# Performance work log

Measured on AMD Instinct MI355X. Metric: run time of the kernel, lower is better.

Reference implementation:

```python
import jax, jax.numpy as jnp
import numpy as np

N, E = 50000, 800000
D, H, C, ED = 128, 8, 16, 4  # embed_dim, heads, head_dim, edge_dim


def _add_self_loops(edge_index, ea, n):
    # PyG add_self_loops with fill_value='mean': self-loop edge_attr is the
    # mean of incoming edge attributes per destination node (0 if none).
    src, dst = edge_index[0], edge_index[1]
    deg = jax.ops.segment_sum(jnp.ones((src.shape[0],), ea.dtype), dst, num_segments=n)
    loop_ea = jax.ops.segment_sum(ea, dst, num_segments=n) / jnp.maximum(deg, 1.0)[:, None]
    ar = jnp.arange(n, dtype=src.dtype)
    return (jnp.concatenate([src, ar]), jnp.concatenate([dst, ar]),
            jnp.concatenate([ea, loop_ea], axis=0))


def _gatv2(x, src, dst, ea, Wl, bl, Wr, br, We, att, bias, concat):
    n = x.shape[0]
    xl = (x @ Wl + bl).reshape(n, H, C)   # lin_l -> messages (source)
    xr = (x @ Wr + br).reshape(n, H, C)   # lin_r -> target
    e = (ea @ We).reshape(-1, H, C)       # lin_edge (no bias in PyG)
    m = jax.nn.leaky_relu(xl[src] + xr[dst] + e, negative_slope=0.2)  # [Etot,H,C]
    alpha = jnp.einsum('ehc,hc->eh', m, att)
    amax = jax.ops.segment_max(alpha, dst, num_segments=n)   # every node has a self loop
    ex = jnp.exp(alpha - amax[dst])
    den = jax.ops.segment_sum(ex, dst, num_segments=n)
    a = ex / den[dst]                                        # segment softmax over dst
    out = jax.ops.segment_sum(xl[src] * a[:, :, None], dst, num_segments=n)  # [N,H,C]
    out = out.reshape(n, H * C) if concat else out.mean(axis=1)
    return out + bias


def _ln(h, g, b):
    mu = h.mean(-1, keepdims=True)
    var = jnp.var(h, axis=-1, keepdims=True)
    return (h - mu) / jnp.sqrt(var + 1e-5) * g + b


def setup_inputs() -> dict:
    key = jax.random.key(0)
    ks = jax.random.split(key, 32)
    s = 0.05
    inp = {
        'x': jax.random.normal(ks[0], (N, D), jnp.float32),
        'edge_index': jax.random.randint(ks[1], (2, E), 0, N, jnp.int32),
        'edge_attr': jax.random.normal(ks[2], (E, ED), jnp.float32),
    }
    dims = [(D, H * C), (H * C, H * C), (H * C, C)]  # (in_dim, bias_dim per layer)
    k = 3
    for i, (din, bdim) in enumerate(dims):
        inp[f'Wl{i}'] = jax.random.normal(ks[k], (din, H * C), jnp.float32) * s; k += 1
        inp[f'bl{i}'] = jnp.zeros((H * C,), jnp.float32)
        inp[f'Wr{i}'] = jax.random.normal(ks[k], (din, H * C), jnp.float32) * s; k += 1
        inp[f'br{i}'] = jnp.zeros((H * C,), jnp.float32)
        inp[f'We{i}'] = jax.random.normal(ks[k], (ED, H * C), jnp.float32) * s; k += 1
        inp[f'att{i}'] = jax.random.normal(ks[k], (H, C), jnp.float32) * s; k += 1
        inp[f'b{i}'] = jnp.zeros((bdim,), jnp.float32)
        inp[f'g{i}'] = jnp.ones((bdim,), jnp.float32)
        inp[f'be{i}'] = jnp.zeros((bdim,), jnp.float32)
    inp['Wout'] = jax.random.normal(ks[k], (C, D), jnp.float32) * s
    inp['bout'] = jnp.zeros((D,), jnp.float32)
    return inp


def reference(x, edge_index, edge_attr,
              Wl0, bl0, Wr0, br0, We0, att0, b0, g0, be0,
              Wl1, bl1, Wr1, br1, We1, att1, b1, g1, be1,
              Wl2, bl2, Wr2, br2, We2, att2, b2, g2, be2,
              Wout, bout):
    n = x.shape[0]
    src, dst, ea = _add_self_loops(edge_index, edge_attr, n)
    layers = [
        (Wl0, bl0, Wr0, br0, We0, att0, b0, g0, be0, True),
        (Wl1, bl1, Wr1, br1, We1, att1, b1, g1, be1, True),
        (Wl2, bl2, Wr2, br2, We2, att2, b2, g2, be2, False),
    ]
    for (Wl, bl, Wr, br, We, att, bias, g, be, concat) in layers:
        h = _gatv2(x, src, dst, ea, Wl, bl, Wr, br, We, att, bias, concat)
        h = jax.nn.elu(h)
        h = _ln(h, g, be)
        if h.shape == x.shape:  # residual (layers 0,1)
            h = h + x
        x = h
    return x @ Wout + bout
```

## Files before the change

kernel.cpp:

```cpp
#include <hip/hip_runtime.h>
#include <hip/hip_bf16.h>

#define ND 128
#define NH 8
#define NC 16

typedef float v2f __attribute__((ext_vector_type(2)));
typedef short bf16x8 __attribute__((ext_vector_type(8)));
typedef float f32x4 __attribute__((ext_vector_type(4)));

static inline size_t alignup(size_t x){ return (x + 255) & ~size_t(255); }

__device__ __forceinline__ ushort f2bf(float f){
    __hip_bfloat16 h = __float2bfloat16(f);
    return *reinterpret_cast<ushort*>(&h);
}

__device__ __forceinline__ v2f unpack_bf2(uint u){
    v2f r;
    r.x = __uint_as_float(u << 16);
    r.y = __uint_as_float(u & 0xffff0000u);
    return r;
}

__device__ __forceinline__ v2f lrelu2(v2f z){
    v2f s = z * 0.2f;
    v2f r;
    r.x = fmaxf(z.x, s.x);
    r.y = fmaxf(z.y, s.y);
    return r;
}

__device__ __forceinline__ float hred8(float x){
    int y;
    y = __builtin_amdgcn_mov_dpp(__float_as_int(x), 0xB1, 0xF, 0xF, true);
    x += __int_as_float(y);
    y = __builtin_amdgcn_mov_dpp(__float_as_int(x), 0x4E, 0xF, 0xF, true);
    x += __int_as_float(y);
    y = __builtin_amdgcn_mov_dpp(__float_as_int(x), 0x141, 0xF, 0xF, true);
    x += __int_as_float(y);
    return x;
}


__global__ void hist_kernel(const int* __restrict__ dsts, int* __restrict__ deg, int E)
{
    int e = blockIdx.x * blockDim.x + threadIdx.x;
    if (e >= E) return;
    atomicAdd(&deg[dsts[e]], 1);
}

__global__ __launch_bounds__(1024) void scan_kernel(const int* __restrict__ deg,
                                                    int* __restrict__ rowstart, int n)
{
    __shared__ int wsum[16];
    int tid = threadIdx.x;
    int lane = tid & 63, wid = tid >> 6;
    int carry = 0;
    for (int base = 0; base < n; base += 4096) {
        int idx = base + tid * 4;
        int4 d = make_int4(0, 0, 0, 0);
        if (idx + 3 < n) d = *(const int4*)(deg + idx);
        else {
            if (idx < n)     d.x = deg[idx];
            if (idx + 1 < n) d.y = deg[idx + 1];
            if (idx + 2 < n) d.z = deg[idx + 2];
        }
        int p0 = (d.x + 3) & ~3, p1 = (d.y + 3) & ~3;
        int p2 = (d.z + 3) & ~3, p3 = (d.w + 3) & ~3;
        int tsum = p0 + p1 + p2 + p3;
        int s = tsum;
        #pragma unroll
        for (int o = 1; o < 64; o <<= 1) {
            int t = __shfl_up(s, o);
            if (lane >= o) s += t;
        }
        if (lane == 63) wsum[wid] = s;
        __syncthreads();
        int off = carry;
        #pragma unroll
        for (int w = 0; w < 16; ++w) {
            int ws_ = wsum[w];
            if (w < wid) off += ws_;
        }
        int total = 0;
        #pragma unroll
        for (int w = 0; w < 16; ++w) total += wsum[w];
        int excl = off + (s - tsum);
        if (idx < n)     rowstart[idx]     = excl;
        if (idx + 1 < n) rowstart[idx + 1] = excl + p0;
        if (idx + 2 < n) rowstart[idx + 2] = excl + p0 + p1;
        if (idx + 3 < n) rowstart[idx + 3] = excl + p0 + p1 + p2;
        carry += total;
        __syncthreads();
    }
    if (tid == 0) rowstart[n] = carry;
}

__global__ void scatter_kernel(const int* __restrict__ srcs, const int* __restrict__ dsts,
                               const float4* __restrict__ ea4,
                               const int* __restrict__ rowstart, int* __restrict__ cursor,
                               int* __restrict__ srcb_sorted, uint2* __restrict__ eab_sorted, int E)
{
    int e = blockIdx.x * blockDim.x + threadIdx.x;
    if (e >= E) return;
    int d = dsts[e];
    int pos = rowstart[d] + atomicAdd(&cursor[d], 1);
    srcb_sorted[pos] = srcs[e] << 8;
    float4 a = ea4[e];
    uint2 p;
    p.x = (uint)f2bf(a.x) | ((uint)f2bf(a.y) << 16);
    p.y = (uint)f2bf(a.z) | ((uint)f2bf(a.w) << 16);
    eab_sorted[pos] = p;
}

__global__ void padfill_kernel(const int* __restrict__ rowstart, const int* __restrict__ deg,
                               int* __restrict__ srcb_sorted, uint2* __restrict__ eab_sorted, int n)
{
    int v = blockIdx.x * blockDim.x + threadIdx.x;
    if (v < n) {
        int d = deg[v];
        int p = rowstart[v] + d;
        int pe = rowstart[v] + ((d + 3) & ~3);
        for (; p < pe; ++p) {
            srcb_sorted[p] = 0;
            eab_sorted[p] = make_uint2(0u, 0u);
        }
    } else if (v < n + 64) {
        int p = rowstart[n] + (v - n);
        srcb_sorted[p] = 0;
        eab_sorted[p] = make_uint2(0u, 0u);
    }
}

__global__ void easum_kernel(const int* __restrict__ rowstart, const int* __restrict__ deg,
                             const uint2* __restrict__ eab_sorted, float4* __restrict__ easum, int n)
{
    int v = blockIdx.x * blockDim.x + threadIdx.x;
    if (v >= n) return;
    int p0 = rowstart[v], d = deg[v];
    float sx = 0.f, sy = 0.f, sz = 0.f, sw = 0.f;
    for (int p = p0; p < p0 + d; ++p) {
        uint2 a = eab_sorted[p];
        sx += __uint_as_float(a.x << 16);
        sy += __uint_as_float(a.x & 0xffff0000u);
        sz += __uint_as_float(a.y << 16);
        sw += __uint_as_float(a.y & 0xffff0000u);
    }
    float inv = 1.0f / (float)(d > 0 ? d : 1);
    easum[v] = make_float4(sx * inv, sy * inv, sz * inv, sw * inv);
}


struct WSrc { const float* p[6]; };

__global__ void wconv_kernel(WSrc s, ushort* __restrict__ wt)
{
    int id = blockIdx.x * blockDim.x + threadIdx.x;
    int m = id >> 14;
    int r = id & 16383;
    int n = r >> 7, k = r & 127;
    wt[(size_t)m * 16384 + n * 128 + k] = f2bf(s.p[m][k * 128 + n]);
}


__global__ __launch_bounds__(256) void gemm_mfma(
    const float* __restrict__ X,
    const ushort* __restrict__ WTl, const float* __restrict__ bl,
    const ushort* __restrict__ WTr, const float* __restrict__ br,
    ushort* __restrict__ XLB, ushort* __restrict__ XRB, int nrows)
{
    __shared__ ushort xhi[64][136];
    __shared__ ushort xlo[64][136];
    int tid = threadIdx.x;
    int row0 = blockIdx.x * 64;

    const float4* X4 = (const float4*)X;
    #pragma unroll
    for (int i = tid; i < 64*32; i += 256) {
        int r = i >> 5, c = i & 31;
        float4 v = make_float4(0.f, 0.f, 0.f, 0.f);
        if (row0 + r < nrows) v = X4[(size_t)(row0 + r) * 32 + c];
        ushort4 h, l;
        h.x = f2bf(v.x); l.x = f2bf(v.x - __uint_as_float((uint)h.x << 16));
        h.y = f2bf(v.y); l.y = f2bf(v.y - __uint_as_float((uint)h.y << 16));
        h.z = f2bf(v.z); l.z = f2bf(v.z - __uint_as_float((uint)h.z << 16));
        h.w = f2bf(v.w); l.w = f2bf(v.w - __uint_as_float((uint)h.w << 16));
        *(ushort4*)&xhi[r][c * 4] = h;
        *(ushort4*)&xlo[r][c * 4] = l;
    }
    __syncthreads();

    int lane = tid & 63;
    int wid = tid >> 6;
    int c15 = lane & 15;
    int kblk = lane >> 4;
    int rowb = wid * 16;

    f32x4 accl[8], accr[8];
    #pragma unroll
    for (int nt = 0; nt < 8; ++nt) {
        float bvl = bl[nt * 16 + c15];
        float bvr = br[nt * 16 + c15];
        accl[nt] = (f32x4){bvl, bvl, bvl, bvl};
        accr[nt] = (f32x4){bvr, bvr, bvr, bvr};
    }

    const bf16x8* WL8 = (const bf16x8*)WTl;
    const bf16x8* WR8 = (const bf16x8*)WTr;

    #pragma unroll
    for (int kc = 0; kc < 4; ++kc) {
        int k0 = kc * 32 + kblk * 8;
        bf16x8 ahi = *(const bf16x8*)&xhi[rowb + c15][k0];
        bf16x8 alo = *(const bf16x8*)&xlo[rowb + c15][k0];
        int kidx = k0 >> 3;
        #pragma unroll
        for (int nt = 0; nt < 8; ++nt) {
            int bi = (nt * 16 + c15) * 16 + kidx;
            bf16x8 bfl = WL8[bi];
            bf16x8 bfr = WR8[bi];
            accl[nt] = __builtin_amdgcn_mfma_f32_16x16x32_bf16(ahi, bfl, accl[nt], 0, 0, 0);
            accl[nt] = __builtin_amdgcn_mfma_f32_16x16x32_bf16(alo, bfl, accl[nt], 0, 0, 0);
            accr[nt] = __builtin_amdgcn_mfma_f32_16x16x32_bf16(ahi, bfr, accr[nt], 0, 0, 0);
            accr[nt] = __builtin_amdgcn_mfma_f32_16x16x32_bf16(alo, bfr, accr[nt], 0, 0, 0);
        }
    }

    int crow = rowb + (lane >> 4) * 4;
    #pragma unroll
    for (int j = 0; j < 4; ++j) {
        int row = row0 + crow + j;
        if (row < nrows) {
            #pragma unroll
            for (int nt = 0; nt < 8; ++nt) {
                XLB[(size_t)row * 128 + nt * 16 + c15] = f2bf(accl[nt][j]);
                XRB[(size_t)row * 128 + nt * 16 + c15] = f2bf(accr[nt][j]);
            }
        }
    }
}


__device__ __forceinline__ void gat_wave(
    int dstv, int t,
    const uint* __restrict__ xl_u, const uint* __restrict__ xr_u,
    const int* __restrict__ rowstart, const int* __restrict__ deg,
    const int* __restrict__ srcb_sorted, const uint2* __restrict__ eab_sorted,
    const float4* __restrict__ easum,
    const float* __restrict__ We, const float* __restrict__ att,
    v2f& r_out, float& l_out)
{
    v2f we0  = ((const v2f*)(We))[t];
    v2f we1  = ((const v2f*)(We + ND))[t];
    v2f we2  = ((const v2f*)(We + 2*ND))[t];
    v2f we3  = ((const v2f*)(We + 3*ND))[t];
    v2f attv = ((const v2f*)att)[t] * 1.44269504f;
    v2f xrv  = unpack_bf2(xr_u[(((uint)dstv) << 6) + t]);

    int p0 = __builtin_amdgcn_readfirstlane(rowstart[dstv]);
    int dv = __builtin_amdgcn_readfirstlane(deg[dstv]);
    int nb = (dv + 3) >> 2;

    uint xsw = xl_u[(((uint)dstv) << 6) + t];

    const int* sp = srcb_sorted + p0;
    const uint4* ebp = (const uint4*)(eab_sorted + p0);
    const char* xlc = (const char*)xl_u;
    uint t4 = (uint)t * 4u;

    v2f a = {0.f, 0.f};
    float lsum = 0.f;

    int4 s0 = *(const int4*)(sp);
    uint xA0 = *(const uint*)(xlc + ((uint)s0.x + t4));
    uint xA1 = *(const uint*)(xlc + ((uint)s0.y + t4));
    uint xA2 = *(const uint*)(xlc + ((uint)s0.z + t4));
    uint xA3 = *(const uint*)(xlc + ((uint)s0.w + t4));
    int4 s1 = *(const int4*)(sp + 4);
    uint xB0 = *(const uint*)(xlc + ((uint)s1.x + t4));
    uint xB1 = *(const uint*)(xlc + ((uint)s1.y + t4));
    uint xB2 = *(const uint*)(xlc + ((uint)s1.z + t4));
    uint xB3 = *(const uint*)(xlc + ((uint)s1.w + t4));
    int4 s2 = *(const int4*)(sp + 8);
    uint xC0 = *(const uint*)(xlc + ((uint)s2.x + t4));
    uint xC1 = *(const uint*)(xlc + ((uint)s2.y + t4));
    uint xC2 = *(const uint*)(xlc + ((uint)s2.z + t4));
    uint xC3 = *(const uint*)(xlc + ((uint)s2.w + t4));
    int4 s3 = *(const int4*)(sp + 12);
    uint4 eA = ebp[0];
    uint4 eB = ebp[1];

    for (int ib = 0; ib < nb; ++ib) {
        uint xD0 = *(const uint*)(xlc + ((uint)s3.x + t4));
        uint xD1 = *(const uint*)(xlc + ((uint)s3.y + t4));
        uint xD2 = *(const uint*)(xlc + ((uint)s3.z + t4));
        uint xD3 = *(const uint*)(xlc + ((uint)s3.w + t4));
        int4 s4 = *(const int4*)(sp + ib*4 + 16);
        uint4 eNA = ebp[(ib + 1) * 2];
        uint4 eNB = ebp[(ib + 1) * 2 + 1];

        float e0x = __uint_as_float(eA.x << 16), e0y = __uint_as_float(eA.x & 0xffff0000u);
        float e0z = __uint_as_float(eA.y << 16), e0w = __uint_as_float(eA.y & 0xffff0000u);
        float e1x = __uint_as_float(eA.z << 16), e1y = __uint_as_float(eA.z & 0xffff0000u);
        float e1z = __uint_as_float(eA.w << 16), e1w = __uint_as_float(eA.w & 0xffff0000u);
        float e2x = __uint_as_float(eB.x << 16), e2y = __uint_as_float(eB.x & 0xffff0000u);
        float e2z = __uint_as_float(eB.y << 16), e2w = __uint_as_float(eB.y & 0xffff0000u);
        float e3x = __uint_as_float(eB.z << 16), e3y = __uint_as_float(eB.z & 0xffff0000u);
        float e3z = __uint_as_float(eB.w << 16), e3w = __uint_as_float(eB.w & 0xffff0000u);

        v2f b0 = xrv + we0*e0x + we1*e0y + we2*e0z + we3*e0w;
        v2f b1 = xrv + we0*e1x + we1*e1y + we2*e1z + we3*e1w;
        v2f b2 = xrv + we0*e2x + we1*e2y + we2*e2z + we3*e2w;
        v2f b3 = xrv + we0*e3x + we1*e3y + we2*e3z + we3*e3w;

        v2f x0 = unpack_bf2(xA0);
        v2f x1 = unpack_bf2(xA1);
        v2f x2 = unpack_bf2(xA2);
        v2f x3 = unpack_bf2(xA3);

        v2f l0 = lrelu2(x0 + b0);
        v2f l1 = lrelu2(x1 + b1);
        v2f l2 = lrelu2(x2 + b2);
        v2f l3 = lrelu2(x3 + b3);

        v2f q0 = l0 * attv;
        v2f q1 = l1 * attv;
        v2f q2 = l2 * attv;
        v2f q3 = l3 * attv;
        float pt0 = q0.x + q0.y;
        float pt1 = q1.x + q1.y;
        float pt2 = q2.x + q2.y;
        float pt3 = q3.x + q3.y;

        if (ib == nb - 1) {
            int live = dv - ib*4;
            pt1 = (live > 1) ? pt1 : -1e30f;
            pt2 = (live > 2) ? pt2 : -1e30f;
            pt3 = (live > 3) ? pt3 : -1e30f;
        }

        float al0 = hred8(pt0);
        float al1 = hred8(pt1);
        float al2 = hred8(pt2);
        float al3 = hred8(pt3);

        float pe0 = exp2f(al0);
        float pe1 = exp2f(al1);
        float pe2 = exp2f(al2);
        float pe3 = exp2f(al3);
        lsum += (pe0 + pe1) + (pe2 + pe3);
        a += x0 * pe0;
        a += x1 * pe1;
        a += x2 * pe2;
        a += x3 * pe3;

        xA0 = xB0; xA1 = xB1; xA2 = xB2; xA3 = xB3;
        xB0 = xC0; xB1 = xC1; xB2 = xC2; xB3 = xC3;
        xC0 = xD0; xC1 = xD1; xC2 = xD2; xC3 = xD3;
        s3 = s4;
        eA = eNA; eB = eNB;
    }

    float4 em = easum[dstv];
    v2f xs = unpack_bf2(xsw);
    v2f bs = xrv + we0*em.x + we1*em.y + we2*em.z + we3*em.w;
    v2f ls = lrelu2(xs + bs);
    v2f qs = ls * attv;
    float al = hred8(qs.x + qs.y);
    float pe = exp2f(al);
    l_out = lsum + pe;
    r_out = a + xs * pe;
}

__global__ __launch_bounds__(256) void attn_concat(
    const ushort* __restrict__ xlb, const ushort* __restrict__ xrb,
    const float* __restrict__ xin,
    const int* __restrict__ rowstart, const int* __restrict__ deg,
    const int* __restrict__ srcb_sorted, const uint2* __restrict__ eab_sorted,
    const float4* __restrict__ easum,
    const float* __restrict__ We, const float* __restrict__ att,
    const float* __restrict__ bias, const float* __restrict__ g, const float* __restrict__ be,
    float* __restrict__ out, int n)
{
    int wid = threadIdx.x >> 6;
    int t = threadIdx.x & 63;
    int dstv = blockIdx.x * 4 + wid;
    if (dstv >= n) return;

    v2f av; float l;
    gat_wave(dstv, t, (const uint*)xlb, (const uint*)xrb, rowstart, deg, srcb_sorted,
             eab_sorted, easum, We, att, av, l);

    v2f bv = ((const v2f*)bias)[t];
    float linv = 1.0f / l;
    v2f h = av * linv + bv;
    h.x = h.x > 0.f ? h.x : (__expf(h.x) - 1.0f);
    h.y = h.y > 0.f ? h.y : (__expf(h.y) - 1.0f);

    float ss = h.x + h.y, qq = h.x*h.x + h.y*h.y;
    #pragma unroll
    for (int o = 1; o < 64; o <<= 1) { ss += __shfl_xor(ss, o); qq += __shfl_xor(qq, o); }
    float mu = ss * (1.0f / ND);
    float var = qq * (1.0f / ND) - mu * mu;
    float rstd = rsqrtf(var + 1e-5f);

    v2f gv  = ((const v2f*)g)[t];
    v2f bev = ((const v2f*)be)[t];
    v2f xiv = ((const v2f*)(xin + (size_t)dstv * ND))[t];
    v2f o2 = (h - mu) * rstd * gv + bev + xiv;
    ((v2f*)(out + (size_t)dstv * ND))[t] = o2;
}

__global__ __launch_bounds__(256) void attn_final(
    const ushort* __restrict__ xlb, const ushort* __restrict__ xrb,
    const int* __restrict__ rowstart, const int* __restrict__ deg,
    const int* __restrict__ srcb_sorted, const uint2* __restrict__ eab_sorted,
    const float4* __restrict__ easum,
    const float* __restrict__ We, const float* __restrict__ att,
    const float* __restrict__ b2, const float* __restrict__ g2, const float* __restrict__ be2,
    const float* __restrict__ Wout, const float* __restrict__ bout,
    float* __restrict__ out, int n)
{
    __shared__ float h16s[4][16];
    int wid = threadIdx.x >> 6;
    int t = threadIdx.x & 63;
    int dstv = blockIdx.x * 4 + wid;
    if (dstv >= n) return;

    v2f av; float l;
    gat_wave(dstv, t, (const uint*)xlb, (const uint*)xrb, rowstart, deg, srcb_sorted,
             eab_sorted, easum, We, att, av, l);
    float linv = 1.0f / l;
    float v0 = av.x * linv, v1 = av.y * linv;

    #pragma unroll
    for (int o = 8; o < 64; o <<= 1) { v0 += __shfl_xor(v0, o); v1 += __shfl_xor(v1, o); }
    int cc = t & 7;
    float2 b2v = ((const float2*)b2)[cc];
    v0 = v0 * (1.0f / NH) + b2v.x;
    v1 = v1 * (1.0f / NH) + b2v.y;
    v0 = v0 > 0.f ? v0 : (__expf(v0) - 1.0f);
    v1 = v1 > 0.f ? v1 : (__expf(v1) - 1.0f);

    float ss = v0 + v1, qq = v0*v0 + v1*v1;
    #pragma unroll
    for (int o = 1; o < 8; o <<= 1) { ss += __shfl_xor(ss, o); qq += __shfl_xor(qq, o); }
    float mu = ss * (1.0f / NC);
    float var = qq * (1.0f / NC) - mu * mu;
    float rstd = rsqrtf(var + 1e-5f);
    float2 g2v = ((const float2*)g2)[cc];
    float2 be2v = ((const float2*)be2)[cc];
    float t0 = (v0 - mu) * rstd * g2v.x + be2v.x;
    float t1 = (v1 - mu) * rstd * g2v.y + be2v.y;

    if (t < 8) { h16s[wid][2*t] = t0; h16s[wid][2*t + 1] = t1; }

    float2 ov = ((const float2*)bout)[t];
    #pragma unroll
    for (int k = 0; k < NC; k++) {
        float hk = h16s[wid][k];
        float2 wv = ((const float2*)Wout)[k * 64 + t];
        ov.x = fmaf(hk, wv.x, ov.x);
        ov.y = fmaf(hk, wv.y, ov.y);
    }
    ((float2*)(out + (size_t)dstv * ND))[t] = ov;
}


extern "C" void kernel_launch(void* const* d_in, const int* in_sizes, int n_in,
                              void* d_out, int out_size, void* d_ws, size_t ws_size,
                              hipStream_t stream)
{
    const float* x_in = (const float*)d_in[0];
    const int*   ei   = (const int*)d_in[1];
    const float* ea   = (const float*)d_in[2];
    const int N = in_sizes[0] / ND;
    const int E = in_sizes[1] / 2;
    const int* srcs = ei;
    const int* dsts = ei + E;
    const float4* ea4 = (const float4*)ea;

    const float *Wl[3], *bl[3], *Wr[3], *br[3], *We[3], *att[3], *bb[3], *gg[3], *be[3];
    for (int l = 0; l < 3; l++) {
        int b = 3 + 9 * l;
        Wl[l]  = (const float*)d_in[b + 0];
        bl[l]  = (const float*)d_in[b + 1];
        Wr[l]  = (const float*)d_in[b + 2];
        br[l]  = (const float*)d_in[b + 3];
        We[l]  = (const float*)d_in[b + 4];
        att[l] = (const float*)d_in[b + 5];
        bb[l]  = (const float*)d_in[b + 6];
        gg[l]  = (const float*)d_in[b + 7];
        be[l]  = (const float*)d_in[b + 8];
    }
    const float* Wout = (const float*)d_in[30];
    const float* bout = (const float*)d_in[31];

    const size_t EP = (size_t)E + 3 * (size_t)N + 96;

    char* ws = (char*)d_ws;
    size_t off = 0;
    int* deg        = (int*)(ws + off);      off = alignup(off + (size_t)N * 4);
    int* cursor     = (int*)(ws + off);      off = alignup(off + (size_t)N * 4);
    size_t zero_bytes = off;
    int* rowstart   = (int*)(ws + off);      off = alignup(off + (size_t)(N + 1) * 4);
    int* srcb_sorted = (int*)(ws + off);     off = alignup(off + EP * 4);
    uint2* eab_sorted = (uint2*)(ws + off);  off = alignup(off + EP * 8);
    float4* easum   = (float4*)(ws + off);   off = alignup(off + (size_t)N * 16);
    ushort* xlb     = (ushort*)(ws + off);   off = alignup(off + (size_t)N * ND * 2);
    ushort* xrb     = (ushort*)(ws + off);   off = alignup(off + (size_t)N * ND * 2);
    float* xa       = (float*)(ws + off);    off = alignup(off + (size_t)N * ND * 4);
    ushort* wt      = (ushort*)(ws + off);   off = alignup(off + (size_t)6 * 16384 * 2);
    float* xb       = (float*)d_out;

    hipMemsetAsync(d_ws, 0, zero_bytes, stream);

    WSrc wsrc;
    wsrc.p[0] = Wl[0]; wsrc.p[1] = Wr[0];
    wsrc.p[2] = Wl[1]; wsrc.p[3] = Wr[1];
    wsrc.p[4] = Wl[2]; wsrc.p[5] = Wr[2];
    wconv_kernel<<<(6 * 16384) / 256, 256, 0, stream>>>(wsrc, wt);

    int ethreads = 256;
    int eblocks = (E + ethreads - 1) / ethreads;
    hist_kernel<<<eblocks, ethreads, 0, stream>>>(dsts, deg, E);
    scan_kernel<<<1, 1024, 0, stream>>>(deg, rowstart, N);
    padfill_kernel<<<(N + 64 + 255) / 256, 256, 0, stream>>>(rowstart, deg, srcb_sorted, eab_sorted, N);
    scatter_kernel<<<eblocks, ethreads, 0, stream>>>(srcs, dsts, ea4, rowstart, cursor,
                                                     srcb_sorted, eab_sorted, E);
    easum_kernel<<<(N + 255) / 256, 256, 0, stream>>>(rowstart, deg, eab_sorted, easum, N);

    int gblocks = (N + 63) / 64;
    int ablocks = (N + 3) / 4;

    const ushort* WT0l = wt;
    const ushort* WT0r = wt + 16384;
    const ushort* WT1l = wt + 2 * 16384;
    const ushort* WT1r = wt + 3 * 16384;
    const ushort* WT2l = wt + 4 * 16384;
    const ushort* WT2r = wt + 5 * 16384;

    gemm_mfma<<<gblocks, 256, 0, stream>>>(x_in, WT0l, bl[0], WT0r, br[0], xlb, xrb, N);
    attn_concat<<<ablocks, 256, 0, stream>>>(xlb, xrb, x_in, rowstart, deg, srcb_sorted, eab_sorted,
                                             easum, We[0], att[0], bb[0], gg[0], be[0], xa, N);
    gemm_mfma<<<gblocks, 256, 0, stream>>>(xa, WT1l, bl[1], WT1r, br[1], xlb, xrb, N);
    attn_concat<<<ablocks, 256, 0, stream>>>(xlb, xrb, xa, rowstart, deg, srcb_sorted, eab_sorted,
                                             easum, We[1], att[1], bb[1], gg[1], be[1], xb, N);
    gemm_mfma<<<gblocks, 256, 0, stream>>>(xb, WT2l, bl[2], WT2r, br[2], xlb, xrb, N);
    attn_final<<<ablocks, 256, 0, stream>>>(xlb, xrb, rowstart, deg, srcb_sorted, eab_sorted,
                                            easum, We[2], att[2], bb[2], gg[2], be[2],
                                            Wout, bout, (float*)d_out, N);
}
```

Baseline: 420.0 us.

## Pack edge records into uint4 AoS and make attention kernels persistent grid-stride

Merges the separate sorted source-index and bf16 edge-attribute arrays into a single 16-byte record per edge, so each edge's source and attributes arrive in one vector load. The gather pipeline is rewritten around these records, with prefetch indices clamped to the last block instead of reading into padding. The attention kernels become persistent: a fixed grid of 2048 blocks strides over nodes and hoists the per-lane weight, att, bias and norm parameter loads out of the node loop. The cost is a larger edge buffer (16 bytes per edge versus 12) that includes an unused word, plus clamping arithmetic in the inner loop.

```diff
diff --git a/kernel.cpp b/kernel.cpp
--- a/kernel.cpp
+++ b/kernel.cpp
@@ -10,6 +10,7 @@
 typedef float f32x4 __attribute__((ext_vector_type(4)));
 
 static inline size_t alignup(size_t x){ return (x + 255) & ~size_t(255); }
+__device__ __forceinline__ int imin(int a, int b){ return a < b ? a : b; }
 
 __device__ __forceinline__ ushort f2bf(float f){
     __hip_bfloat16 h = __float2bfloat16(f);
@@ -100,52 +101,46 @@
 __global__ void scatter_kernel(const int* __restrict__ srcs, const int* __restrict__ dsts,
                                const float4* __restrict__ ea4,
                                const int* __restrict__ rowstart, int* __restrict__ cursor,
-                               int* __restrict__ srcb_sorted, uint2* __restrict__ eab_sorted, int E)
+                               uint4* __restrict__ recs, int E)
 {
     int e = blockIdx.x * blockDim.x + threadIdx.x;
     if (e >= E) return;
     int d = dsts[e];
     int pos = rowstart[d] + atomicAdd(&cursor[d], 1);
-    srcb_sorted[pos] = srcs[e] << 8;
     float4 a = ea4[e];
-    uint2 p;
-    p.x = (uint)f2bf(a.x) | ((uint)f2bf(a.y) << 16);
-    p.y = (uint)f2bf(a.z) | ((uint)f2bf(a.w) << 16);
-    eab_sorted[pos] = p;
+    uint ea01 = (uint)f2bf(a.x) | ((uint)f2bf(a.y) << 16);
+    uint ea23 = (uint)f2bf(a.z) | ((uint)f2bf(a.w) << 16);
+    recs[pos] = make_uint4((uint)(srcs[e] << 8), ea01, ea23, 0u);
 }
 
 __global__ void padfill_kernel(const int* __restrict__ rowstart, const int* __restrict__ deg,
-                               int* __restrict__ srcb_sorted, uint2* __restrict__ eab_sorted, int n)
+                               uint4* __restrict__ recs, int n)
 {
     int v = blockIdx.x * blockDim.x + threadIdx.x;
     if (v < n) {
         int d = deg[v];
         int p = rowstart[v] + d;
         int pe = rowstart[v] + ((d + 3) & ~3);
-        for (; p < pe; ++p) {
-            srcb_sorted[p] = 0;
-            eab_sorted[p] = make_uint2(0u, 0u);
-        }
+        for (; p < pe; ++p) recs[p] = make_uint4(0u, 0u, 0u, 0u);
     } else if (v < n + 64) {
         int p = rowstart[n] + (v - n);
-        srcb_sorted[p] = 0;
-        eab_sorted[p] = make_uint2(0u, 0u);
+        recs[p] = make_uint4(0u, 0u, 0u, 0u);
     }
 }
 
 __global__ void easum_kernel(const int* __restrict__ rowstart, const int* __restrict__ deg,
-                             const uint2* __restrict__ eab_sorted, float4* __restrict__ easum, int n)
+                             const uint4* __restrict__ recs, float4* __restrict__ easum, int n)
 {
     int v = blockIdx.x * blockDim.x + threadIdx.x;
     if (v >= n) return;
     int p0 = rowstart[v], d = deg[v];
     float sx = 0.f, sy = 0.f, sz = 0.f, sw = 0.f;
     for (int p = p0; p < p0 + d; ++p) {
-        uint2 a = eab_sorted[p];
-        sx += __uint_as_float(a.x << 16);
-        sy += __uint_as_float(a.x & 0xffff0000u);
-        sz += __uint_as_float(a.y << 16);
-        sw += __uint_as_float(a.y & 0xffff0000u);
+        uint4 a = recs[p];
+        sx += __uint_as_float(a.y << 16);
+        sy += __uint_as_float(a.y & 0xffff0000u);
+        sz += __uint_as_float(a.z << 16);
+        sw += __uint_as_float(a.z & 0xffff0000u);
     }
     float inv = 1.0f / (float)(d > 0 ? d : 1);
     easum[v] = make_float4(sx * inv, sy * inv, sz * inv, sw * inv);
@@ -246,78 +241,66 @@
     int dstv, int t,
     const uint* __restrict__ xl_u, const uint* __restrict__ xr_u,
     const int* __restrict__ rowstart, const int* __restrict__ deg,
-    const int* __restrict__ srcb_sorted, const uint2* __restrict__ eab_sorted,
-    const float4* __restrict__ easum,
-    const float* __restrict__ We, const float* __restrict__ att,
+    const uint4* __restrict__ recs, const float4* __restrict__ easum,
+    v2f we0, v2f we1, v2f we2, v2f we3, v2f attv,
     v2f& r_out, float& l_out)
 {
-    v2f we0  = ((const v2f*)(We))[t];
-    v2f we1  = ((const v2f*)(We + ND))[t];
-    v2f we2  = ((const v2f*)(We + 2*ND))[t];
-    v2f we3  = ((const v2f*)(We + 3*ND))[t];
-    v2f attv = ((const v2f*)att)[t] * 1.44269504f;
-    v2f xrv  = unpack_bf2(xr_u[(((uint)dstv) << 6) + t]);
-
+    v2f xrv = unpack_bf2(xr_u[(((uint)dstv) << 6) + t]);
     int p0 = __builtin_amdgcn_readfirstlane(rowstart[dstv]);
     int dv = __builtin_amdgcn_readfirstlane(deg[dstv]);
     int nb = (dv + 3) >> 2;
+    int nbm1 = nb > 0 ? nb - 1 : 0;
 
     uint xsw = xl_u[(((uint)dstv) << 6) + t];
 
-    const int* sp = srcb_sorted + p0;
-    const uint4* ebp = (const uint4*)(eab_sorted + p0);
+    const uint4* rp = recs + p0;
     const char* xlc = (const char*)xl_u;
     uint t4 = (uint)t * 4u;
 
     v2f a = {0.f, 0.f};
     float lsum = 0.f;
 
-    int4 s0 = *(const int4*)(sp);
-    uint xA0 = *(const uint*)(xlc + ((uint)s0.x + t4));
-    uint xA1 = *(const uint*)(xlc + ((uint)s0.y + t4));
-    uint xA2 = *(const uint*)(xlc + ((uint)s0.z + t4));
-    uint xA3 = *(const uint*)(xlc + ((uint)s0.w + t4));
-    int4 s1 = *(const int4*)(sp + 4);
-    uint xB0 = *(const uint*)(xlc + ((uint)s1.x + t4));
-    uint xB1 = *(const uint*)(xlc + ((uint)s1.y + t4));
-    uint xB2 = *(const uint*)(xlc + ((uint)s1.z + t4));
-    uint xB3 = *(const uint*)(xlc + ((uint)s1.w + t4));
-    int4 s2 = *(const int4*)(sp + 8);
-    uint xC0 = *(const uint*)(xlc + ((uint)s2.x + t4));
-    uint xC1 = *(const uint*)(xlc + ((uint)s2.y + t4));
-    uint xC2 = *(const uint*)(xlc + ((uint)s2.z + t4));
-    uint xC3 = *(const uint*)(xlc + ((uint)s2.w + t4));
-    int4 s3 = *(const int4*)(sp + 12);
-    uint4 eA = ebp[0];
-    uint4 eB = ebp[1];
+    uint4 rA0 = rp[0], rA1 = rp[1], rA2 = rp[2], rA3 = rp[3];
+    int i1 = imin(1, nbm1) * 4;
+    uint4 rB0 = rp[i1], rB1 = rp[i1+1], rB2 = rp[i1+2], rB3 = rp[i1+3];
+    int i2 = imin(2, nbm1) * 4;
+    uint4 rC0 = rp[i2], rC1 = rp[i2+1], rC2 = rp[i2+2], rC3 = rp[i2+3];
+
+    uint gA0 = *(const uint*)(xlc + (rA0.x + t4));
+    uint gA1 = *(const uint*)(xlc + (rA1.x + t4));
+    uint gA2 = *(const uint*)(xlc + (rA2.x + t4));
+    uint gA3 = *(const uint*)(xlc + (rA3.x + t4));
+    uint gB0 = *(const uint*)(xlc + (rB0.x + t4));
+    uint gB1 = *(const uint*)(xlc + (rB1.x + t4));
+    uint gB2 = *(const uint*)(xlc + (rB2.x + t4));
+    uint gB3 = *(const uint*)(xlc + (rB3.x + t4));
 
     for (int ib = 0; ib < nb; ++ib) {
-        uint xD0 = *(const uint*)(xlc + ((uint)s3.x + t4));
-        uint xD1 = *(const uint*)(xlc + ((uint)s3.y + t4));
-        uint xD2 = *(const uint*)(xlc + ((uint)s3.z + t4));
-        uint xD3 = *(const uint*)(xlc + ((uint)s3.w + t4));
-        int4 s4 = *(const int4*)(sp + ib*4 + 16);
-        uint4 eNA = ebp[(ib + 1) * 2];
-        uint4 eNB = ebp[(ib + 1) * 2 + 1];
-
-        float e0x = __uint_as_float(eA.x << 16), e0y = __uint_as_float(eA.x & 0xffff0000u);
-        float e0z = __uint_as_float(eA.y << 16), e0w = __uint_as_float(eA.y & 0xffff0000u);
-        float e1x = __uint_as_float(eA.z << 16), e1y = __uint_as_float(eA.z & 0xffff0000u);
-        float e1z = __uint_as_float(eA.w << 16), e1w = __uint_as_float(eA.w & 0xffff0000u);
-        float e2x = __uint_as_float(eB.x << 16), e2y = __uint_as_float(eB.x & 0xffff0000u);
-        float e2z = __uint_as_float(eB.y << 16), e2w = __uint_as_float(eB.y & 0xffff0000u);
-        float e3x = __uint_as_float(eB.z << 16), e3y = __uint_as_float(eB.z & 0xffff0000u);
-        float e3z = __uint_as_float(eB.w << 16), e3w = __uint_as_float(eB.w & 0xffff0000u);
+        uint gC0 = *(const uint*)(xlc + (rC0.x + t4));
+        uint gC1 = *(const uint*)(xlc + (rC1.x + t4));
+        uint gC2 = *(const uint*)(xlc + (rC2.x + t4));
+        uint gC3 = *(const uint*)(xlc + (rC3.x + t4));
+        int i3 = imin(ib + 3, nbm1) * 4;
+        uint4 rD0 = rp[i3], rD1 = rp[i3+1], rD2 = rp[i3+2], rD3 = rp[i3+3];
+
+        float e0x = __uint_as_float(rA0.y << 16), e0y = __uint_as_float(rA0.y & 0xffff0000u);
+        float e0z = __uint_as_float(rA0.z << 16), e0w = __uint_as_float(rA0.z & 0xffff0000u);
+        float e1x = __uint_as_float(rA1.y << 16), e1y = __uint_as_float(rA1.y & 0xffff0000u);
+        float e1z = __uint_as_float(rA1.z << 16), e1w = __uint_as_float(rA1.z & 0xffff0000u);
+        float e2x = __uint_as_float(rA2.y << 16), e2y = __uint_as_float(rA2.y & 0xffff0000u);
+        float e2z = __uint_as_float(rA2.z << 16), e2w = __uint_as_float(rA2.z & 0xffff0000u);
+        float e3x = __uint_as_float(rA3.y << 16), e3y = __uint_as_float(rA3.y & 0xffff0000u);
+        float e3z = __uint_as_float(rA3.z << 16), e3w = __uint_as_float(rA3.z & 0xffff0000u);
 
         v2f b0 = xrv + we0*e0x + we1*e0y + we2*e0z + we3*e0w;
         v2f b1 = xrv + we0*e1x + we1*e1y + we2*e1z + we3*e1w;
         v2f b2 = xrv + we0*e2x + we1*e2y + we2*e2z + we3*e2w;
         v2f b3 = xrv + we0*e3x + we1*e3y + we2*e3z + we3*e3w;
 
-        v2f x0 = unpack_bf2(xA0);
-        v2f x1 = unpack_bf2(xA1);
-        v2f x2 = unpack_bf2(xA2);
-        v2f x3 = unpack_bf2(xA3);
+        v2f x0 = unpack_bf2(gA0);
+        v2f x1 = unpack_bf2(gA1);
+        v2f x2 = unpack_bf2(gA2);
+        v2f x3 = unpack_bf2(gA3);
 
         v2f l0 = lrelu2(x0 + b0);
         v2f l1 = lrelu2(x1 + b1);
@@ -355,11 +338,11 @@
         a += x2 * pe2;
         a += x3 * pe3;
 
-        xA0 = xB0; xA1 = xB1; xA2 = xB2; xA3 = xB3;
-        xB0 = xC0; xB1 = xC1; xB2 = xC2; xB3 = xC3;
-        xC0 = xD0; xC1 = xD1; xC2 = xD2; xC3 = xD3;
-        s3 = s4;
-        eA = eNA; eB = eNB;
+        gA0 = gB0; gA1 = gB1; gA2 = gB2; gA3 = gB3;
+        gB0 = gC0; gB1 = gC1; gB2 = gC2; gB3 = gC3;
+        rA0 = rB0; rA1 = rB1; rA2 = rB2; rA3 = rB3;
+        rB0 = rC0; rB1 = rC1; rB2 = rC2; rB3 = rC3;
+        rC0 = rD0; rC1 = rD1; rC2 = rD2; rC3 = rD3;
     }
 
     float4 em = easum[dstv];
@@ -377,94 +360,105 @@
     const ushort* __restrict__ xlb, const ushort* __restrict__ xrb,
     const float* __restrict__ xin,
     const int* __restrict__ rowstart, const int* __restrict__ deg,
-    const int* __restrict__ srcb_sorted, const uint2* __restrict__ eab_sorted,
-    const float4* __restrict__ easum,
+    const uint4* __restrict__ recs, const float4* __restrict__ easum,
     const float* __restrict__ We, const float* __restrict__ att,
     const float* __restrict__ bias, const float* __restrict__ g, const float* __restrict__ be,
-    float* __restrict__ out, int n)
+    float* __restrict__ out, int n, int stride)
 {
     int wid = threadIdx.x >> 6;
     int t = threadIdx.x & 63;
-    int dstv = blockIdx.x * 4 + wid;
-    if (dstv >= n) return;
-
-    v2f av; float l;
-    gat_wave(dstv, t, (const uint*)xlb, (const uint*)xrb, rowstart, deg, srcb_sorted,
-             eab_sorted, easum, We, att, av, l);
-
-    v2f bv = ((const v2f*)bias)[t];
-    float linv = 1.0f / l;
-    v2f h = av * linv + bv;
-    h.x = h.x > 0.f ? h.x : (__expf(h.x) - 1.0f);
-    h.y = h.y > 0.f ? h.y : (__expf(h.y) - 1.0f);
-
-    float ss = h.x + h.y, qq = h.x*h.x + h.y*h.y;
-    #pragma unroll
-    for (int o = 1; o < 64; o <<= 1) { ss += __shfl_xor(ss, o); qq += __shfl_xor(qq, o); }
-    float mu = ss * (1.0f / ND);
-    float var = qq * (1.0f / ND) - mu * mu;
-    float rstd = rsqrtf(var + 1e-5f);
-
-    v2f gv  = ((const v2f*)g)[t];
-    v2f bev = ((const v2f*)be)[t];
-    v2f xiv = ((const v2f*)(xin + (size_t)dstv * ND))[t];
-    v2f o2 = (h - mu) * rstd * gv + bev + xiv;
-    ((v2f*)(out + (size_t)dstv * ND))[t] = o2;
+
+    v2f we0  = ((const v2f*)(We))[t];
+    v2f we1  = ((const v2f*)(We + ND))[t];
+    v2f we2  = ((const v2f*)(We + 2*ND))[t];
+    v2f we3  = ((const v2f*)(We + 3*ND))[t];
+    v2f attv = ((const v2f*)att)[t] * 1.44269504f;
+    v2f bv   = ((const v2f*)bias)[t];
+    v2f gv   = ((const v2f*)g)[t];
+    v2f bev  = ((const v2f*)be)[t];
+
+    for (int dstv = blockIdx.x * 4 + wid; dstv < n; dstv += stride) {
+        v2f av; float l;
+        gat_wave(dstv, t, (const uint*)xlb, (const uint*)xrb, rowstart, deg, recs, easum,
+                 we0, we1, we2, we3, attv, av, l);
+
+        float linv = 1.0f / l;
+        v2f h = av * linv + bv;
+        h.x = h.x > 0.f ? h.x : (__expf(h.x) - 1.0f);
+        h.y = h.y > 0.f ? h.y : (__expf(h.y) - 1.0f);
+
+        float ss = h.x + h.y, qq = h.x*h.x + h.y*h.y;
+        #pragma unroll
+        for (int o = 1; o < 64; o <<= 1) { ss += __shfl_xor(ss, o); qq += __shfl_xor(qq, o); }
+        float mu = ss * (1.0f / ND);
+        float var = qq * (1.0f / ND) - mu * mu;
+        float rstd = rsqrtf(var + 1e-5f);
+
+        v2f xiv = ((const v2f*)(xin + (size_t)dstv * ND))[t];
+        v2f o2 = (h - mu) * rstd * gv + bev + xiv;
+        ((v2f*)(out + (size_t)dstv * ND))[t] = o2;
+    }
 }
 
 __global__ __launch_bounds__(256) void attn_final(
     const ushort* __restrict__ xlb, const ushort* __restrict__ xrb,
     const int* __restrict__ rowstart, const int* __restrict__ deg,
-    const int* __restrict__ srcb_sorted, const uint2* __restrict__ eab_sorted,
-    const float4* __restrict__ easum,
+    const uint4* __restrict__ recs, const float4* __restrict__ easum,
     const float* __restrict__ We, const float* __restrict__ att,
     const float* __restrict__ b2, const float* __restrict__ g2, const float* __restrict__ be2,
     const float* __restrict__ Wout, const float* __restrict__ bout,
-    float* __restrict__ out, int n)
+    float* __restrict__ out, int n, int stride)
 {
     __shared__ float h16s[4][16];
     int wid = threadIdx.x >> 6;
     int t = threadIdx.x & 63;
-    int dstv = blockIdx.x * 4 + wid;
-    if (dstv >= n) return;
-
-    v2f av; float l;
-    gat_wave(dstv, t, (const uint*)xlb, (const uint*)xrb, rowstart, deg, srcb_sorted,
-             eab_sorted, easum, We, att, av, l);
-    float linv = 1.0f / l;
-    float v0 = av.x * linv, v1 = av.y * linv;
-
-    #pragma unroll
-    for (int o = 8; o < 64; o <<= 1) { v0 += __shfl_xor(v0, o); v1 += __shfl_xor(v1, o); }
+
+    v2f we0  = ((const v2f*)(We))[t];
+    v2f we1  = ((const v2f*)(We + ND))[t];
+    v2f we2  = ((const v2f*)(We + 2*ND))[t];
+    v2f we3  = ((const v2f*)(We + 3*ND))[t];
+    v2f attv = ((const v2f*)att)[t] * 1.44269504f;
     int cc = t & 7;
-    float2 b2v = ((const float2*)b2)[cc];
-    v0 = v0 * (1.0f / NH) + b2v.x;
-    v1 = v1 * (1.0f / NH) + b2v.y;
-    v0 = v0 > 0.f ? v0 : (__expf(v0) - 1.0f);
-    v1 = v1 > 0.f ? v1 : (__expf(v1) - 1.0f);
-
-    float ss = v0 + v1, qq = v0*v0 + v1*v1;
-    #pragma unroll
-    for (int o = 1; o < 8; o <<= 1) { ss += __shfl_xor(ss, o); qq += __shfl_xor(qq, o); }
-    float mu = ss * (1.0f / NC);
-    float var = qq * (1.0f / NC) - mu * mu;
-    float rstd = rsqrtf(var + 1e-5f);
-    float2 g2v = ((const float2*)g2)[cc];
+    float2 b2v  = ((const float2*)b2)[cc];
+    float2 g2v  = ((const float2*)g2)[cc];
     float2 be2v = ((const float2*)be2)[cc];
-    float t0 = (v0 - mu) * rstd * g2v.x + be2v.x;
-    float t1 = (v1 - mu) * rstd * g2v.y + be2v.y;
-
-    if (t < 8) { h16s[wid][2*t] = t0; h16s[wid][2*t + 1] = t1; }
-
-    float2 ov = ((const float2*)bout)[t];
-    #pragma unroll
-    for (int k = 0; k < NC; k++) {
-        float hk = h16s[wid][k];
-        float2 wv = ((const float2*)Wout)[k * 64 + t];
-        ov.x = fmaf(hk, wv.x, ov.x);
-        ov.y = fmaf(hk, wv.y, ov.y);
-    }
-    ((float2*)(out + (size_t)dstv * ND))[t] = ov;
+    float2 ov0  = ((const float2*)bout)[t];
+
+    for (int dstv = blockIdx.x * 4 + wid; dstv < n; dstv += stride) {
+        v2f av; float l;
+        gat_wave(dstv, t, (const uint*)xlb, (const uint*)xrb, rowstart, deg, recs, easum,
+                 we0, we1, we2, we3, attv, av, l);
+        float linv = 1.0f / l;
+        float v0 = av.x * linv, v1 = av.y * linv;
+
+        #pragma unroll
+        for (int o = 8; o < 64; o <<= 1) { v0 += __shfl_xor(v0, o); v1 += __shfl_xor(v1, o); }
+        v0 = v0 * (1.0f / NH) + b2v.x;
+        v1 = v1 * (1.0f / NH) + b2v.y;
+        v0 = v0 > 0.f ? v0 : (__expf(v0) - 1.0f);
+        v1 = v1 > 0.f ? v1 : (__expf(v1) - 1.0f);
+
+        float ss = v0 + v1, qq = v0*v0 + v1*v1;
+        #pragma unroll
+        for (int o = 1; o < 8; o <<= 1) { ss += __shfl_xor(ss, o); qq += __shfl_xor(qq, o); }
+        float mu = ss * (1.0f / NC);
+        float var = qq * (1.0f / NC) - mu * mu;
+        float rstd = rsqrtf(var + 1e-5f);
+        float t0 = (v0 - mu) * rstd * g2v.x + be2v.x;
+        float t1 = (v1 - mu) * rstd * g2v.y + be2v.y;
+
+        if (t < 8) { h16s[wid][2*t] = t0; h16s[wid][2*t + 1] = t1; }
+
+        float2 ov = ov0;
+        #pragma unroll
+        for (int k = 0; k < NC; k++) {
+            float hk = h16s[wid][k];
+            float2 wv = ((const float2*)Wout)[k * 64 + t];
+            ov.x = fmaf(hk, wv.x, ov.x);
+            ov.y = fmaf(hk, wv.y, ov.y);
+        }
+        ((float2*)(out + (size_t)dstv * ND))[t] = ov;
+    }
 }
 
 
@@ -505,8 +499,7 @@
     int* cursor     = (int*)(ws + off);      off = alignup(off + (size_t)N * 4);
     size_t zero_bytes = off;
     int* rowstart   = (int*)(ws + off);      off = alignup(off + (size_t)(N + 1) * 4);
-    int* srcb_sorted = (int*)(ws + off);     off = alignup(off + EP * 4);
-    uint2* eab_sorted = (uint2*)(ws + off);  off = alignup(off + EP * 8);
+    uint4* recs     = (uint4*)(ws + off);    off = alignup(off + EP * 16);
     float4* easum   = (float4*)(ws + off);   off = alignup(off + (size_t)N * 16);
     ushort* xlb     = (ushort*)(ws + off);   off = alignup(off + (size_t)N * ND * 2);
     ushort* xrb     = (ushort*)(ws + off);   off = alignup(off + (size_t)N * ND * 2);
@@ -526,13 +519,13 @@
     int eblocks = (E + ethreads - 1) / ethreads;
     hist_kernel<<<eblocks, ethreads, 0, stream>>>(dsts, deg, E);
     scan_kernel<<<1, 1024, 0, stream>>>(deg, rowstart, N);
-    padfill_kernel<<<(N + 64 + 255) / 256, 256, 0, stream>>>(rowstart, deg, srcb_sorted, eab_sorted, N);
-    scatter_kernel<<<eblocks, ethreads, 0, stream>>>(srcs, dsts, ea4, rowstart, cursor,
-                                                     srcb_sorted, eab_sorted, E);
-    easum_kernel<<<(N + 255) / 256, 256, 0, stream>>>(rowstart, deg, eab_sorted, easum, N);
+    padfill_kernel<<<(N + 64 + 255) / 256, 256, 0, stream>>>(rowstart, deg, recs, N);
+    scatter_kernel<<<eblocks, ethreads, 0, stream>>>(srcs, dsts, ea4, rowstart, cursor, recs, E);
+    easum_kernel<<<(N + 255) / 256, 256, 0, stream>>>(rowstart, deg, recs, easum, N);
 
     int gblocks = (N + 63) / 64;
-    int ablocks = (N + 3) / 4;
+    int ablocks = 2048;
+    int astride = ablocks * 4;
 
     const ushort* WT0l = wt;
     const ushort* WT0r = wt + 16384;
@@ -542,13 +535,13 @@
     const ushort* WT2r = wt + 5 * 16384;
 
     gemm_mfma<<<gblocks, 256, 0, stream>>>(x_in, WT0l, bl[0], WT0r, br[0], xlb, xrb, N);
-    attn_concat<<<ablocks, 256, 0, stream>>>(xlb, xrb, x_in, rowstart, deg, srcb_sorted, eab_sorted,
-                                             easum, We[0], att[0], bb[0], gg[0], be[0], xa, N);
+    attn_concat<<<ablocks, 256, 0, stream>>>(xlb, xrb, x_in, rowstart, deg, recs, easum,
+                                             We[0], att[0], bb[0], gg[0], be[0], xa, N, astride);
     gemm_mfma<<<gblocks, 256, 0, stream>>>(xa, WT1l, bl[1], WT1r, br[1], xlb, xrb, N);
-    attn_concat<<<ablocks, 256, 0, stream>>>(xlb, xrb, xa, rowstart, deg, srcb_sorted, eab_sorted,
-                                             easum, We[1], att[1], bb[1], gg[1], be[1], xb, N);
+    attn_concat<<<ablocks, 256, 0, stream>>>(xlb, xrb, xa, rowstart, deg, recs, easum,
+                                             We[1], att[1], bb[1], gg[1], be[1], xb, N, astride);
     gemm_mfma<<<gblocks, 256, 0, stream>>>(xb, WT2l, bl[2], WT2r, br[2], xlb, xrb, N);
-    attn_final<<<ablocks, 256, 0, stream>>>(xlb, xrb, rowstart, deg, srcb_sorted, eab_sorted,
-                                            easum, We[2], att[2], bb[2], gg[2], be[2],
-                                            Wout, bout, (float*)d_out, N);
-}
+    attn_final<<<ablocks, 256, 0, stream>>>(xlb, xrb, rowstart, deg, recs, easum,
+                                            We[2], att[2], bb[2], gg[2], be[2],
+                                            Wout, bout, (float*)d_out, N, astride);
+}
```

New measurement: 450.8 us. 7.3% more time.
